# Performance work log

Hardware: AMD Instinct MI355X
Metric: run time of the kernel (lower is better)

## Reference

```python
import jax, jax.numpy as jnp
import numpy as np

N_NODES = 100000
N_EDGES = 1000000
N_RELS = 8
N_HEADS = 4
IN_FEAT = 64
OUT_FEAT = 64
D_HEAD = OUT_FEAT // N_HEADS
LEAKY_SLOPE = 0.2


def setup_inputs() -> dict:
    key = jax.random.key(0)
    ks = jax.random.split(key, 8)
    x = jax.random.normal(ks[0], (N_NODES, IN_FEAT), dtype=jnp.float32)
    src_idx = jax.random.randint(ks[1], (N_EDGES,), 0, N_NODES)
    dst_idx = jax.random.randint(ks[2], (N_EDGES,), 0, N_NODES)
    edge_rel = jnp.sort(jax.random.randint(ks[3], (N_EDGES,), 0, N_RELS))
    # xavier-ish small init for weights
    conv_weights = jax.random.normal(ks[4], (N_RELS, N_HEADS, IN_FEAT, D_HEAD), dtype=jnp.float32) * 0.1
    attn_l = jax.random.normal(ks[5], (N_RELS, N_HEADS, D_HEAD), dtype=jnp.float32) * 0.1
    attn_r = jax.random.normal(ks[6], (N_RELS, N_HEADS, D_HEAD), dtype=jnp.float32) * 0.1
    h_bias = jnp.zeros((OUT_FEAT,), dtype=jnp.float32)
    return {
        'x': x, 'src_idx': src_idx, 'dst_idx': dst_idx, 'edge_rel': edge_rel,
        'conv_weights': conv_weights, 'attn_l': attn_l, 'attn_r': attn_r,
        'h_bias': h_bias,
    }


def reference(x, src_idx, dst_idx, edge_rel, conv_weights, attn_l, attn_r, h_bias):
    N = x.shape[0]
    # Per-relation transform of all node features: [R, N, H, D]
    feat_all = jnp.einsum('ni,rhid->rnhd', x, conv_weights)
    # Per-relation attention logits per node: [R, N, H]
    el_all = jnp.einsum('rnhd,rhd->rnh', feat_all, attn_l)
    er_all = jnp.einsum('rnhd,rhd->rnh', feat_all, attn_r)
    # Gather per-edge quantities (relation-specific transform of src/dst)
    feat_e = feat_all[edge_rel, src_idx]          # [E, H, D]
    el = el_all[edge_rel, src_idx]                # [E, H]
    er = er_all[edge_rel, dst_idx]                # [E, H]
    s = jax.nn.leaky_relu(el + er, negative_slope=LEAKY_SLOPE)
    # Edge softmax over incoming edges of each destination node (per head)
    m = jax.ops.segment_max(s, dst_idx, num_segments=N)      # [N, H]
    e = jnp.exp(s - m[dst_idx])                               # [E, H]
    denom = jax.ops.segment_sum(e, dst_idx, num_segments=N)   # [N, H]
    w = e / jnp.maximum(denom[dst_idx], jnp.float32(1e-16))   # [E, H]
    # Weighted aggregation of source features into destination nodes
    agg = jax.ops.segment_sum(feat_e * w[..., None], dst_idx, num_segments=N)  # [N, H, D]
    h = agg.reshape(N, OUT_FEAT) + h_bias
    # activation=None, dropout in eval mode -> identity
    return h
```

## Files before the change

kernel.cpp:

```cpp
#include <hip/hip_runtime.h>
#include <hip/hip_bf16.h>

#define NN 100000
#define NE 1000000
#define NR 8

#define EB 4096
#define NBLK 245
#define NBUCK 196
#define NT (NBUCK*NBLK)
#define NBB 188

typedef unsigned short u16;
typedef unsigned int u32;
typedef __attribute__((ext_vector_type(8))) short bf16x8;
typedef __attribute__((ext_vector_type(4))) float f32x4;

static __device__ __forceinline__ float bf2f(u16 u) {
    union { u32 i; float f; } v; v.i = ((u32)u) << 16; return v.f;
}
static __device__ __forceinline__ u16 f2bf(float f) {
    __hip_bfloat16 h = __float2bfloat16(f);
    return *reinterpret_cast<u16*>(&h);
}
static __device__ __forceinline__ float ldf(const void* p, int idx, int isf32) {
    return isf32 ? ((const float*)p)[idx] : bf2f(((const u16*)p)[idx]);
}

__global__ void k_detect(const u16* __restrict__ xw, int* __restrict__ flag)
{
    int t = threadIdx.x;
    int insane = 0;
    for (int k = t; k < 512; k += 64) {
        u16 w = xw[k];
        int ex = (w >> 7) & 0xFF;
        bool sane = ((w & 0x7FFF) == 0) || (ex >= 96 && ex <= 159);
        insane += sane ? 0 : 1;
    }
    for (int off = 32; off; off >>= 1) insane += __shfl_down(insane, off);
    if (t == 0) *flag = (insane > 50) ? 1 : 0;
}

__global__ void k_cvt(const void* __restrict__ xin, const int* __restrict__ flag,
                      u16* __restrict__ xb)
{
    int i = blockIdx.x * blockDim.x + threadIdx.x;
    if (i >= NN * 8) return;
    if (*flag) {
        const float* xf = (const float*)xin;
        u16 o[8];
#pragma unroll
        for (int j = 0; j < 8; ++j) o[j] = f2bf(xf[i * 8 + j]);
        uint4 v;
        v.x = (u32)o[0] | ((u32)o[1] << 16);
        v.y = (u32)o[2] | ((u32)o[3] << 16);
        v.z = (u32)o[4] | ((u32)o[5] << 16);
        v.w = (u32)o[6] | ((u32)o[7] << 16);
        ((uint4*)xb)[i] = v;
    } else {
        ((uint4*)xb)[i] = ((const uint4*)xin)[i];
    }
}

__global__ void k0_prep(const void* __restrict__ cw, const void* __restrict__ al,
                        const void* __restrict__ ar, const int* __restrict__ flag,
                        u16* __restrict__ Bpre)
{
    int tid = blockIdx.x * blockDim.x + threadIdx.x;
    if (tid >= NR * 5120) return;
    int isf32 = *flag;
    int r = tid / 5120, rem = tid % 5120;
    int c = rem >> 3, j = rem & 7;
    int nt = c >> 7, kk = (c >> 6) & 1, lc = c & 63;
    int i = kk * 32 + ((lc >> 4) << 3) + j;
    int d = lc & 15;
    u16 val;
    if (nt < 4) {
        val = f2bf(ldf(cw, ((r * 4 + nt) * 64 + i) * 16 + d, isf32));
    } else if (d < 8) {
        int h = d >> 1;
        const void* attn = (d & 1) ? ar : al;
        float s = 0.f;
        for (int dd = 0; dd < 16; ++dd)
            s += ldf(cw, ((r * 4 + h) * 64 + i) * 16 + dd, isf32)
               * ldf(attn, (r * 4 + h) * 16 + dd, isf32);
        val = f2bf(s);
    } else {
        val = 0;
    }
    Bpre[tid] = val;
}

__global__ __launch_bounds__(256) void k1_feat(
    const u16* __restrict__ xb, const u16* __restrict__ Bpre,
    u16* __restrict__ feat_all, float* __restrict__ el_all, float* __restrict__ er_all)
{
    __shared__ alignas(16) u16 ldsA[4096];
    __shared__ alignas(16) u16 ldsB[5120];
    int n0 = blockIdx.x * 64;
    int r = blockIdx.y;
    int tid = threadIdx.x;
    int wave = tid >> 6, lane = tid & 63;

    for (int c = tid; c < 512; c += 256) {
        int mt = c >> 7, kk = (c >> 6) & 1, lc = c & 63;
        int node = n0 + mt * 16 + (lc & 15);
        if (node >= NN) node = NN - 1;
        int kbase = kk * 32 + ((lc >> 4) << 3);
        *(uint4*)&ldsA[c * 8] = *(const uint4*)&xb[node * 64 + kbase];
    }
    for (int c = tid; c < 640; c += 256)
        *(uint4*)&ldsB[c * 8] = *(const uint4*)&Bpre[r * 5120 + c * 8];
    __syncthreads();

    bf16x8 afrag0 = *(bf16x8*)&ldsA[((wave * 2 + 0) * 64 + lane) * 8];
    bf16x8 afrag1 = *(bf16x8*)&ldsA[((wave * 2 + 1) * 64 + lane) * 8];
    f32x4 acc[5];
#pragma unroll
    for (int nt = 0; nt < 5; ++nt) acc[nt] = f32x4{0.f, 0.f, 0.f, 0.f};
#pragma unroll
    for (int nt = 0; nt < 5; ++nt) {
        bf16x8 b0 = *(bf16x8*)&ldsB[((nt * 2 + 0) * 64 + lane) * 8];
        bf16x8 b1 = *(bf16x8*)&ldsB[((nt * 2 + 1) * 64 + lane) * 8];
        acc[nt] = __builtin_amdgcn_mfma_f32_16x16x32_bf16(afrag0, b0, acc[nt], 0, 0, 0);
        acc[nt] = __builtin_amdgcn_mfma_f32_16x16x32_bf16(afrag1, b1, acc[nt], 0, 0, 0);
    }

    int col = lane & 15, quad = lane >> 4;
    if (col < 8) {
        int h = col >> 1;
        float* dstp = (col & 1) ? er_all : el_all;
#pragma unroll
        for (int reg = 0; reg < 4; ++reg) {
            int node = n0 + wave * 16 + quad * 4 + reg;
            if (node < NN) dstp[(r * NN + node) * 4 + h] = acc[4][reg];
        }
    }
    __syncthreads();
#pragma unroll
    for (int nt = 0; nt < 4; ++nt) {
        int cg = nt * 16 + col;
#pragma unroll
        for (int reg = 0; reg < 4; ++reg) {
            int row = quad * 4 + reg;
            ldsA[(wave * 16 + row) * 64 + cg] = f2bf(acc[nt][reg]);
        }
    }
    __syncthreads();
    for (int c = tid; c < 512; c += 256) {
        int nl = c >> 3, part = c & 7;
        int node = n0 + nl;
        if (node < NN)
            *(uint4*)&feat_all[(r * NN + node) * 64 + part * 8] = *(uint4*)&ldsA[c * 8];
    }
}

__global__ __launch_bounds__(256) void k_binA(const int* __restrict__ dsti,
                                              int* __restrict__ histT)
{
    __shared__ int hist[NBUCK];
    int t = threadIdx.x, blk = blockIdx.x;
    if (t < NBUCK) hist[t] = 0;
    __syncthreads();
    int base = blk * EB;
    for (int j = 0; j < EB; j += 256) {
        int e = base + j + t;
        if (e < NE) atomicAdd(&hist[dsti[e] >> 9], 1);
    }
    __syncthreads();
    if (t < NBUCK) histT[t * NBLK + blk] = hist[t];
}

__global__ __launch_bounds__(256) void k_scanB1(int* __restrict__ histT,
                                                int* __restrict__ bsum)
{
    __shared__ int wtot[4];
    int t = threadIdx.x;
    int gi = blockIdx.x * 256 + t;
    int v = (gi < NT) ? histT[gi] : 0;
    int lane = t & 63, w = t >> 6;
    int s = v;
#pragma unroll
    for (int m = 1; m < 64; m <<= 1) {
        int u = __shfl_up(s, m);
        if (lane >= m) s += u;
    }
    if (lane == 63) wtot[w] = s;
    __syncthreads();
    int wb = 0;
    for (int i = 0; i < w; ++i) wb += wtot[i];
    if (gi < NT) histT[gi] = wb + s - v;
    if (t == 255) bsum[blockIdx.x] = wb + s;
}

__global__ __launch_bounds__(256) void k_scanB2(const int* __restrict__ bsum,
                                                int* __restrict__ boff)
{
    __shared__ int wtot[4];
    int t = threadIdx.x;
    int v = (t < NBB) ? bsum[t] : 0;
    int lane = t & 63, w = t >> 6;
    int s = v;
#pragma unroll
    for (int m = 1; m < 64; m <<= 1) {
        int u = __shfl_up(s, m);
        if (lane >= m) s += u;
    }
    if (lane == 63) wtot[w] = s;
    __syncthreads();
    int wb = 0;
    for (int i = 0; i < w; ++i) wb += wtot[i];
    if (t < NBB) boff[t] = wb + s - v;
}

__global__ __launch_bounds__(256) void k_scanB3(const int* __restrict__ boff,
                                                int* __restrict__ histT,
                                                int* __restrict__ bstart)
{
    int gi = blockIdx.x * 256 + threadIdx.x;
    if (gi < NT) {
        int val = histT[gi] + boff[blockIdx.x];
        histT[gi] = val;
        if (gi % NBLK == 0) bstart[gi / NBLK] = val;
    }
    if (gi == 0) bstart[NBUCK] = NE;
}

__global__ __launch_bounds__(256) void k_binC(
    const int* __restrict__ srci, const int* __restrict__ dsti,
    const int* __restrict__ reli, const int* __restrict__ histT,
    int* __restrict__ key_b)
{
    __shared__ int cur[NBUCK];
    int t = threadIdx.x, blk = blockIdx.x;
    if (t < NBUCK) cur[t] = histT[t * NBLK + blk];
    __syncthreads();
    int base = blk * EB;
    for (int j = 0; j < EB; j += 256) {
        int e = base + j + t;
        if (e < NE) {
            int d = dsti[e];
            int key = ((d & 511) << 20) | (reli[e] << 17) | srci[e];
            int pos = atomicAdd(&cur[d >> 9], 1);
            key_b[pos] = key;
        }
    }
}

__global__ __launch_bounds__(512) void k_binD(
    const int* __restrict__ bstart, const int* __restrict__ key_b,
    int* __restrict__ key_s, int* __restrict__ off)
{
    __shared__ int cnt[512];
    __shared__ int wtot[8];
    int t = threadIdx.x, b = blockIdx.x;
    int s0 = bstart[b], s1 = bstart[b + 1];
    cnt[t] = 0;
    __syncthreads();
    for (int j = s0 + t; j < s1; j += 512)
        atomicAdd(&cnt[(key_b[j] >> 20) & 511], 1);
    __syncthreads();
    int v = cnt[t];
    int lane = t & 63, w = t >> 6;
    int s = v;
#pragma unroll
    for (int m = 1; m < 64; m <<= 1) {
        int u = __shfl_up(s, m);
        if (lane >= m) s += u;
    }
    if (lane == 63) wtot[w] = s;
    __syncthreads();
    int wb = 0;
    for (int i = 0; i < w; ++i) wb += wtot[i];
    int excl = s0 + wb + s - v;
    int d = (b << 9) + t;
    if (d < NN) off[d] = excl;
    __syncthreads();
    cnt[t] = excl;
    if (b == 0 && t == 0) off[NN] = NE;
    __syncthreads();
    for (int j = s0 + t; j < s1; j += 512) {
        int key = key_b[j];
        int pos = atomicAdd(&cnt[(key >> 20) & 511], 1);
        key_s[pos] = key;
    }
}

__global__ __launch_bounds__(256) void k3_node(
    const int* __restrict__ off, const int* __restrict__ key_s,
    const float* __restrict__ el_all, const float* __restrict__ er_all,
    const u16* __restrict__ feat_all, const void* __restrict__ bias,
    const int* __restrict__ flag, void* __restrict__ out)
{
    __shared__ int   ldsK[4][64];
    __shared__ float ldsE[4][64][4];
    int wave = threadIdx.x >> 6, lane = threadIdx.x & 63;
    int h = lane >> 4;
    int gw = blockIdx.x * 4 + wave;
    int nw = gridDim.x * 4;
    int isf32 = *flag;
    float bv = ldf(bias, lane, isf32);

    for (int d = gw; d < NN; d += nw) {
        int start = off[d], end = off[d + 1];
        int deg = end - start;

        f32x4 dsum = f32x4{0.f, 0.f, 0.f, 0.f};
        for (int base = 0; base < deg; base += 64) {
            int j = base + lane;
            if (j < deg) {
                int key = key_s[start + j];
                int rel = (key >> 17) & 7, src = key & 131071;
                int kk = rel * NN + src;
                f32x4 el = *(const f32x4*)&el_all[kk * 4];
                f32x4 er = *(const f32x4*)&er_all[(rel * NN + d) * 4];
                f32x4 ee;
#pragma unroll
                for (int q = 0; q < 4; ++q) {
                    float v = el[q] + er[q];
                    v = v > 0.f ? v : 0.2f * v;
                    ee[q] = __expf(v);
                }
                if (base == 0) {
                    ldsK[wave][lane] = kk;
                    *(f32x4*)&ldsE[wave][lane][0] = ee;
                }
                dsum.x += ee.x; dsum.y += ee.y; dsum.z += ee.z; dsum.w += ee.w;
            }
        }
#pragma unroll
        for (int m = 1; m < 64; m <<= 1) {
            dsum.x += __shfl_xor(dsum.x, m);
            dsum.y += __shfl_xor(dsum.y, m);
            dsum.z += __shfl_xor(dsum.z, m);
            dsum.w += __shfl_xor(dsum.w, m);
        }
        float invh = 1.f / fmaxf(h == 0 ? dsum.x : h == 1 ? dsum.y : h == 2 ? dsum.z : dsum.w,
                                 1e-16f);

        float acc = 0.f;
        for (int base = 0; base < deg; base += 64) {
            int cn = min(64, deg - base);
            if (base > 0) {
                int j = base + lane;
                if (lane < cn) {
                    int key = key_s[start + j];
                    int rel = (key >> 17) & 7, src = key & 131071;
                    int kk = rel * NN + src;
                    f32x4 el = *(const f32x4*)&el_all[kk * 4];
                    f32x4 er = *(const f32x4*)&er_all[(rel * NN + d) * 4];
                    f32x4 ee;
#pragma unroll
                    for (int q = 0; q < 4; ++q) {
                        float v = el[q] + er[q];
                        v = v > 0.f ? v : 0.2f * v;
                        ee[q] = __expf(v);
                    }
                    ldsK[wave][lane] = kk;
                    *(f32x4*)&ldsE[wave][lane][0] = ee;
                }
            }
#pragma unroll 4
            for (int e = 0; e < cn; ++e) {
                int k = ldsK[wave][e];
                float w = ldsE[wave][e][h] * invh;
                float fv = bf2f(feat_all[k * 64 + lane]);
                acc += fv * w;
            }
        }
        float o = acc + bv;
        if (isf32) ((float*)out)[d * 64 + lane] = o;
        else       ((u16*)out)[d * 64 + lane] = f2bf(o);
    }
}

extern "C" void kernel_launch(void* const* d_in, const int* in_sizes, int n_in,
                              void* d_out, int out_size, void* d_ws, size_t ws_size,
                              hipStream_t stream)
{
    const void* x   = d_in[0];
    const int* srci = (const int*)d_in[1];
    const int* dsti = (const int*)d_in[2];
    const int* reli = (const int*)d_in[3];
    const void* cw  = d_in[4];
    const void* al  = d_in[5];
    const void* ar  = d_in[6];
    const void* hb  = d_in[7];

    char* ws = (char*)d_ws;
    u16*   feat_all = (u16*)  (ws + 0);
    float* el_all   = (float*)(ws + 102400000);
    float* er_all   = (float*)(ws + 115200000);
    int*   key_s    = (int*)  (ws + 128000000);
    int*   key_b    = (int*)  (ws + 132000000);
    int*   off      = (int*)  (ws + 136000000);
    int*   histT    = (int*)  (ws + 136400064);
    int*   bsum     = (int*)  (ws + 136592192);
    int*   boff     = (int*)  (ws + 136592960);
    int*   bstart   = (int*)  (ws + 136593728);
    u16*   Bpre     = (u16*)  (ws + 136594560);
    u16*   xb       = (u16*)  (ws + 136676480);
    int*   flag     = (int*)  (ws + 149476480);

    k_detect<<<1, 64, 0, stream>>>((const u16*)x, flag);
    k_cvt<<<(NN * 8 + 255) / 256, 256, 0, stream>>>(x, flag, xb);
    k0_prep<<<(NR * 5120 + 255) / 256, 256, 0, stream>>>(cw, al, ar, flag, Bpre);
    k1_feat<<<dim3((NN + 63) / 64, NR), 256, 0, stream>>>(xb, Bpre, feat_all, el_all, er_all);
    k_binA<<<NBLK, 256, 0, stream>>>(dsti, histT);
    k_scanB1<<<NBB, 256, 0, stream>>>(histT, bsum);
    k_scanB2<<<1, 256, 0, stream>>>(bsum, boff);
    k_scanB3<<<NBB, 256, 0, stream>>>(boff, histT, bstart);
    k_binC<<<NBLK, 256, 0, stream>>>(srci, dsti, reli, histT, key_b);
    k_binD<<<NBUCK, 512, 0, stream>>>(bstart, key_b, key_s, off);
    k3_node<<<(NN + 3) / 4, 256, 0, stream>>>(off, key_s, el_all, er_all, feat_all,
                                              hb, flag, d_out);
}
```

Baseline: 232.3 us.

## Precompute per-edge attention exponentials in separate pass; single-pass node aggregation

Adds a kernel that computes exp(leaky_relu(el+er)) for every sorted edge and stores it as a float4 array. The node kernel then reads these precomputed weights, accumulates the unnormalised weighted sum and the denominator in a single pass, and applies the normalisation once at the end. The gather loop is also unrolled by 8 so more feature loads are in flight at once. This removes recomputing exponentials for nodes with degree above 64 and the second pass over edges, at the cost of an extra 16 MB write and read and one more kernel launch.

Measured after the change: 250.3 us. 1.08x slower.

```diff
diff --git a/kernel.cpp b/kernel.cpp
--- a/kernel.cpp
+++ b/kernel.cpp
@@ -286,11 +286,35 @@
     }
 }
 
+__global__ __launch_bounds__(256) void k2e(
+    const int* __restrict__ bstart, const int* __restrict__ key_s,
+    const float* __restrict__ el_all, const float* __restrict__ er_all,
+    f32x4* __restrict__ ew)
+{
+    int b = blockIdx.x;
+    int s0 = bstart[b], s1 = bstart[b + 1];
+    for (int j = s0 + threadIdx.x; j < s1; j += 256) {
+        int key = key_s[j];
+        int rel = (key >> 17) & 7, src = key & 131071;
+        int d = (b << 9) | ((key >> 20) & 511);
+        f32x4 el = *(const f32x4*)&el_all[(rel * NN + src) * 4];
+        f32x4 er = *(const f32x4*)&er_all[(rel * NN + d) * 4];
+        f32x4 ee;
+#pragma unroll
+        for (int q = 0; q < 4; ++q) {
+            float v = el[q] + er[q];
+            v = v > 0.f ? v : 0.2f * v;
+            ee[q] = __expf(v);
+        }
+        ew[j] = ee;
+    }
+}
+
 __global__ __launch_bounds__(256) void k3_node(
     const int* __restrict__ off, const int* __restrict__ key_s,
-    const float* __restrict__ el_all, const float* __restrict__ er_all,
-    const u16* __restrict__ feat_all, const void* __restrict__ bias,
-    const int* __restrict__ flag, void* __restrict__ out)
+    const f32x4* __restrict__ ew, const u16* __restrict__ feat_all,
+    const void* __restrict__ bias, const int* __restrict__ flag,
+    void* __restrict__ out)
 {
     __shared__ int   ldsK[4][64];
     __shared__ float ldsE[4][64][4];
@@ -305,28 +329,32 @@
         int start = off[d], end = off[d + 1];
         int deg = end - start;
 
+        float acc = 0.f;
         f32x4 dsum = f32x4{0.f, 0.f, 0.f, 0.f};
         for (int base = 0; base < deg; base += 64) {
+            int cn = min(64, deg - base);
             int j = base + lane;
-            if (j < deg) {
+            if (lane < cn) {
                 int key = key_s[start + j];
-                int rel = (key >> 17) & 7, src = key & 131071;
-                int kk = rel * NN + src;
-                f32x4 el = *(const f32x4*)&el_all[kk * 4];
-                f32x4 er = *(const f32x4*)&er_all[(rel * NN + d) * 4];
-                f32x4 ee;
-#pragma unroll
-                for (int q = 0; q < 4; ++q) {
-                    float v = el[q] + er[q];
-                    v = v > 0.f ? v : 0.2f * v;
-                    ee[q] = __expf(v);
-                }
-                if (base == 0) {
-                    ldsK[wave][lane] = kk;
-                    *(f32x4*)&ldsE[wave][lane][0] = ee;
-                }
+                ldsK[wave][lane] = ((key >> 17) & 7) * NN + (key & 131071);
+                f32x4 ee = ew[start + j];
+                *(f32x4*)&ldsE[wave][lane][0] = ee;
                 dsum.x += ee.x; dsum.y += ee.y; dsum.z += ee.z; dsum.w += ee.w;
             }
+            int e = 0;
+            for (; e + 8 <= cn; e += 8) {
+                int kk[8]; float fv[8], wv[8];
+#pragma unroll
+                for (int q = 0; q < 8; ++q) kk[q] = ldsK[wave][e + q];
+#pragma unroll
+                for (int q = 0; q < 8; ++q) fv[q] = bf2f(feat_all[kk[q] * 64 + lane]);
+#pragma unroll
+                for (int q = 0; q < 8; ++q) wv[q] = ldsE[wave][e + q][h];
+#pragma unroll
+                for (int q = 0; q < 8; ++q) acc += fv[q] * wv[q];
+            }
+            for (; e < cn; ++e)
+                acc += bf2f(feat_all[ldsK[wave][e] * 64 + lane]) * ldsE[wave][e][h];
         }
 #pragma unroll
         for (int m = 1; m < 64; m <<= 1) {
@@ -337,38 +365,7 @@
         }
         float invh = 1.f / fmaxf(h == 0 ? dsum.x : h == 1 ? dsum.y : h == 2 ? dsum.z : dsum.w,
                                  1e-16f);
-
-        float acc = 0.f;
-        for (int base = 0; base < deg; base += 64) {
-            int cn = min(64, deg - base);
-            if (base > 0) {
-                int j = base + lane;
-                if (lane < cn) {
-                    int key = key_s[start + j];
-                    int rel = (key >> 17) & 7, src = key & 131071;
-                    int kk = rel * NN + src;
-                    f32x4 el = *(const f32x4*)&el_all[kk * 4];
-                    f32x4 er = *(const f32x4*)&er_all[(rel * NN + d) * 4];
-                    f32x4 ee;
-#pragma unroll
-                    for (int q = 0; q < 4; ++q) {
-                        float v = el[q] + er[q];
-                        v = v > 0.f ? v : 0.2f * v;
-                        ee[q] = __expf(v);
-                    }
-                    ldsK[wave][lane] = kk;
-                    *(f32x4*)&ldsE[wave][lane][0] = ee;
-                }
-            }
-#pragma unroll 4
-            for (int e = 0; e < cn; ++e) {
-                int k = ldsK[wave][e];
-                float w = ldsE[wave][e][h] * invh;
-                float fv = bf2f(feat_all[k * 64 + lane]);
-                acc += fv * w;
-            }
-        }
-        float o = acc + bv;
+        float o = acc * invh + bv;
         if (isf32) ((float*)out)[d * 64 + lane] = o;
         else       ((u16*)out)[d * 64 + lane] = f2bf(o);
     }
@@ -393,14 +390,15 @@
     float* er_all   = (float*)(ws + 115200000);
     int*   key_s    = (int*)  (ws + 128000000);
     int*   key_b    = (int*)  (ws + 132000000);
-    int*   off      = (int*)  (ws + 136000000);
-    int*   histT    = (int*)  (ws + 136400064);
-    int*   bsum     = (int*)  (ws + 136592192);
-    int*   boff     = (int*)  (ws + 136592960);
-    int*   bstart   = (int*)  (ws + 136593728);
-    u16*   Bpre     = (u16*)  (ws + 136594560);
-    u16*   xb       = (u16*)  (ws + 136676480);
-    int*   flag     = (int*)  (ws + 149476480);
+    f32x4* ew       = (f32x4*)(ws + 136000000);
+    int*   off      = (int*)  (ws + 152000000);
+    int*   histT    = (int*)  (ws + 152400064);
+    int*   bsum     = (int*)  (ws + 152592192);
+    int*   boff     = (int*)  (ws + 152592960);
+    int*   bstart   = (int*)  (ws + 152593728);
+    u16*   Bpre     = (u16*)  (ws + 152594560);
+    u16*   xb       = (u16*)  (ws + 152676480);
+    int*   flag     = (int*)  (ws + 165476480);
 
     k_detect<<<1, 64, 0, stream>>>((const u16*)x, flag);
     k_cvt<<<(NN * 8 + 255) / 256, 256, 0, stream>>>(x, flag, xb);
@@ -412,6 +410,6 @@
     k_scanB3<<<NBB, 256, 0, stream>>>(boff, histT, bstart);
     k_binC<<<NBLK, 256, 0, stream>>>(srci, dsti, reli, histT, key_b);
     k_binD<<<NBUCK, 512, 0, stream>>>(bstart, key_b, key_s, off);
-    k3_node<<<(NN + 3) / 4, 256, 0, stream>>>(off, key_s, el_all, er_all, feat_all,
-                                              hb, flag, d_out);
-}
+    k2e<<<NBUCK, 256, 0, stream>>>(bstart, key_s, el_all, er_all, ew);
+    k3_node<<<(NN + 3) / 4, 256, 0, stream>>>(off, key_s, ew, feat_all, hb, flag, d_out);
+}
```

## Single-pass node aggregation with deferred normalization and 4-edge parallel gather

Applied to the files above, without the earlier changes.

Merges the two edge passes per destination node into one by accumulating unnormalized weighted features together with the weight sum, and normalizing only at the end. Each wave now handles 4 edges at a time, with 16 lanes per edge and each lane loading 4 bf16 features as one 8-byte load, followed by a cross-group shuffle reduction. This removes the recomputation of logits and exps for high-degree nodes and reduces the number of serial gather iterations. In exchange it adds padded dummy edges that gather row 0 with zero weight and a few extra shuffles per node.

Measured after the change: 231.3 us. Within noise of the previous version (-0.4%).

```diff
diff --git a/kernel.cpp b/kernel.cpp
--- a/kernel.cpp
+++ b/kernel.cpp
@@ -18,6 +18,12 @@
 
 static __device__ __forceinline__ float bf2f(u16 u) {
     union { u32 i; float f; } v; v.i = ((u32)u) << 16; return v.f;
+}
+static __device__ __forceinline__ float bflo(u32 u) {
+    union { u32 i; float f; } v; v.i = u << 16; return v.f;
+}
+static __device__ __forceinline__ float bfhi(u32 u) {
+    union { u32 i; float f; } v; v.i = u & 0xffff0000u; return v.f;
 }
 static __device__ __forceinline__ u16 f2bf(float f) {
     __hip_bfloat16 h = __float2bfloat16(f);
@@ -295,21 +301,26 @@
     __shared__ int   ldsK[4][64];
     __shared__ float ldsE[4][64][4];
     int wave = threadIdx.x >> 6, lane = threadIdx.x & 63;
-    int h = lane >> 4;
+    int eg = lane >> 4;
+    int fl = lane & 15;
+    int h  = fl >> 2;
     int gw = blockIdx.x * 4 + wave;
     int nw = gridDim.x * 4;
     int isf32 = *flag;
-    float bv = ldf(bias, lane, isf32);
+    float bv0 = ldf(bias, fl * 4 + 0, isf32);
+    float bv1 = ldf(bias, fl * 4 + 1, isf32);
+    float bv2 = ldf(bias, fl * 4 + 2, isf32);
+    float bv3 = ldf(bias, fl * 4 + 3, isf32);
 
     for (int d = gw; d < NN; d += nw) {
         int start = off[d], end = off[d + 1];
         int deg = end - start;
 
-        f32x4 dsum = f32x4{0.f, 0.f, 0.f, 0.f};
+        float acc0 = 0.f, acc1 = 0.f, acc2 = 0.f, acc3 = 0.f, accW = 0.f;
         for (int base = 0; base < deg; base += 64) {
-            int j = base + lane;
-            if (j < deg) {
-                int key = key_s[start + j];
+            int cn = min(64, deg - base);
+            if (lane < cn) {
+                int key = key_s[start + base + lane];
                 int rel = (key >> 17) & 7, src = key & 131071;
                 int kk = rel * NN + src;
                 f32x4 el = *(const f32x4*)&el_all[kk * 4];
@@ -321,56 +332,47 @@
                     v = v > 0.f ? v : 0.2f * v;
                     ee[q] = __expf(v);
                 }
-                if (base == 0) {
-                    ldsK[wave][lane] = kk;
-                    *(f32x4*)&ldsE[wave][lane][0] = ee;
-                }
-                dsum.x += ee.x; dsum.y += ee.y; dsum.z += ee.z; dsum.w += ee.w;
+                ldsK[wave][lane] = kk;
+                *(f32x4*)&ldsE[wave][lane][0] = ee;
+            } else {
+                ldsK[wave][lane] = 0;
+                *(f32x4*)&ldsE[wave][lane][0] = f32x4{0.f, 0.f, 0.f, 0.f};
             }
-        }
-#pragma unroll
-        for (int m = 1; m < 64; m <<= 1) {
-            dsum.x += __shfl_xor(dsum.x, m);
-            dsum.y += __shfl_xor(dsum.y, m);
-            dsum.z += __shfl_xor(dsum.z, m);
-            dsum.w += __shfl_xor(dsum.w, m);
-        }
-        float invh = 1.f / fmaxf(h == 0 ? dsum.x : h == 1 ? dsum.y : h == 2 ? dsum.z : dsum.w,
-                                 1e-16f);
-
-        float acc = 0.f;
-        for (int base = 0; base < deg; base += 64) {
-            int cn = min(64, deg - base);
-            if (base > 0) {
-                int j = base + lane;
-                if (lane < cn) {
-                    int key = key_s[start + j];
-                    int rel = (key >> 17) & 7, src = key & 131071;
-                    int kk = rel * NN + src;
-                    f32x4 el = *(const f32x4*)&el_all[kk * 4];
-                    f32x4 er = *(const f32x4*)&er_all[(rel * NN + d) * 4];
-                    f32x4 ee;
-#pragma unroll
-                    for (int q = 0; q < 4; ++q) {
-                        float v = el[q] + er[q];
-                        v = v > 0.f ? v : 0.2f * v;
-                        ee[q] = __expf(v);
-                    }
-                    ldsK[wave][lane] = kk;
-                    *(f32x4*)&ldsE[wave][lane][0] = ee;
-                }
+            int cnr = (cn + 3) & ~3;
+            for (int e = 0; e < cnr; e += 4) {
+                int   ke = ldsK[wave][e + eg];
+                float w  = ldsE[wave][e + eg][h];
+                uint2 u  = *(const uint2*)&feat_all[ke * 64 + fl * 4];
+                acc0 += bflo(u.x) * w;
+                acc1 += bfhi(u.x) * w;
+                acc2 += bflo(u.y) * w;
+                acc3 += bfhi(u.y) * w;
+                accW += w;
             }
-#pragma unroll 4
-            for (int e = 0; e < cn; ++e) {
-                int k = ldsK[wave][e];
-                float w = ldsE[wave][e][h] * invh;
-                float fv = bf2f(feat_all[k * 64 + lane]);
-                acc += fv * w;
+        }
+#pragma unroll
+        for (int m = 16; m < 64; m <<= 1) {
+            acc0 += __shfl_xor(acc0, m);
+            acc1 += __shfl_xor(acc1, m);
+            acc2 += __shfl_xor(acc2, m);
+            acc3 += __shfl_xor(acc3, m);
+            accW += __shfl_xor(accW, m);
+        }
+        float invh = 1.f / fmaxf(accW, 1e-16f);
+        if (eg == 0) {
+            float o0 = acc0 * invh + bv0;
+            float o1 = acc1 * invh + bv1;
+            float o2 = acc2 * invh + bv2;
+            float o3 = acc3 * invh + bv3;
+            if (isf32) {
+                ((f32x4*)out)[d * 16 + fl] = f32x4{o0, o1, o2, o3};
+            } else {
+                uint2 st;
+                st.x = (u32)f2bf(o0) | ((u32)f2bf(o1) << 16);
+                st.y = (u32)f2bf(o2) | ((u32)f2bf(o3) << 16);
+                *(uint2*)&((u16*)out)[d * 64 + fl * 4] = st;
             }
         }
-        float o = acc + bv;
-        if (isf32) ((float*)out)[d * 64 + lane] = o;
-        else       ((u16*)out)[d * 64 + lane] = f2bf(o);
     }
 }
 
```
